# Optimization experiments

Hardware: AMD Instinct MI355X
Metric: run time of the kernel (lower is better)

Reference implementation:

```python
import jax, jax.numpy as jnp
import numpy as np
import math

E = 1024      # embed_dim
H = 16        # num_heads
D = E // H    # head_dim = 64 (power of two, padded_dim == head_dim)


def fwht(x):
    """Normalized fast Walsh-Hadamard transform on last dim (power of two)."""
    n = x.shape[-1]
    orig = x.shape
    x = x.reshape(-1, n)
    h = 1
    while h < n:  # log2(n) fixed butterfly stages
        x = x.reshape(-1, n // (2 * h), 2, h)
        a, b = x[:, :, 0, :], x[:, :, 1, :]
        x = jnp.stack([a + b, a - b], axis=2).reshape(-1, n)
        h *= 2
    return (x / math.sqrt(n)).reshape(orig)


def apply_transform(x, diag, alpha, bias):
    # x: [b, h, s, d]; gated FWHT-domain diagonal filter residual
    x_f = fwht(x) * diag
    x_inv = fwht(x_f)
    return x + alpha * x_inv + bias


def setup_inputs() -> dict:
    key = jax.random.key(0)
    ks = jax.random.split(key, 6)
    b, s = 2, 2048
    sc_in = 1.0 / math.sqrt(E)
    return {
        "x": jax.random.normal(ks[0], (b, s, E), jnp.float32),
        "mask": jnp.ones((b, s), jnp.int32),
        "Wqkv": jax.random.normal(ks[1], (E, 3 * E), jnp.float32) * sc_in,
        "bqkv": jnp.zeros((3 * E,), jnp.float32),
        "Wout": jax.random.normal(ks[2], (E, E), jnp.float32) * sc_in,
        "bout": jnp.zeros((E,), jnp.float32),
        "diag": jnp.ones((D,), jnp.float32) * 0.05,
        "alpha": jnp.float32(0.1),
        "bias_h": jnp.zeros((D,), jnp.float32),
    }


def reference(x, mask, Wqkv, bqkv, Wout, bout, diag, alpha, bias_h):
    b, s, _ = x.shape
    qkv = x @ Wqkv + bqkv                       # [b, s, 3E]
    q, k, v = jnp.split(qkv, 3, axis=-1)

    def to_heads(t):
        return t.reshape(b, s, H, D).transpose(0, 2, 1, 3)  # [b, h, s, d]

    qh, kh, vh = to_heads(q), to_heads(k), to_heads(v)
    qh = apply_transform(qh, diag, alpha, bias_h)
    kh = apply_transform(kh, diag, alpha, bias_h)

    scores = jnp.einsum('bhqd,bhkd->bhqk', qh, kh) / math.sqrt(D)
    scores = jnp.where(mask[:, None, None, :] == 0, -jnp.inf, scores)
    weights = jax.nn.softmax(scores, axis=-1)

    out = jnp.einsum('bhqk,bhkd->bhqd', weights, vh)
    out = out.transpose(0, 2, 1, 3).reshape(b, s, E)
    return out @ Wout + bout
```

## Files before the change

### kernel.cpp

```cpp
#include <hip/hip_runtime.h>
#include <cmath>

#define B_ 2
#define S_ 2048
#define E_ 1024
#define H_ 16
#define M_ (B_*S_)
#define N3_ (3*E_)

typedef unsigned short u16;
typedef unsigned int u32;
typedef __attribute__((ext_vector_type(8))) short bf16x8;
typedef __attribute__((ext_vector_type(8))) _Float16 f16x8;
typedef __attribute__((ext_vector_type(4))) float f32x4;

__device__ __forceinline__ u16 f2bf(float x) {
    unsigned u = __float_as_uint(x);
    return (u16)((u + 0x7FFFu + ((u >> 16) & 1u)) >> 16);
}
__device__ __forceinline__ float bf2f(u16 h) {
    return __uint_as_float((u32)h << 16);
}
__device__ __forceinline__ u16 f2h(float x) {
    _Float16 h = (_Float16)x;
    return __builtin_bit_cast(u16, h);
}
__device__ __forceinline__ float h2f(u16 b) {
    return (float)__builtin_bit_cast(_Float16, b);
}
__device__ __forceinline__ void gld_lds16(const void* g, void* l) {
    __builtin_amdgcn_global_load_lds((const __attribute__((address_space(1))) void*)g,
                                     (__attribute__((address_space(3))) void*)l, 16, 0, 0);
}

template<bool F16>
__device__ __forceinline__ f32x4 mma16(bf16x8 a, bf16x8 b, f32x4 c) {
    if constexpr (F16)
        return __builtin_amdgcn_mfma_f32_16x16x32_f16(
            __builtin_bit_cast(f16x8, a), __builtin_bit_cast(f16x8, b), c, 0, 0, 0);
    else
        return __builtin_amdgcn_mfma_f32_16x16x32_bf16(a, b, c, 0, 0, 0);
}

__global__ __launch_bounds__(256)
void split_a_f16(const float* __restrict__ in, u16* __restrict__ hi, u16* __restrict__ lo, int n4)
{
    int i = blockIdx.x * 256 + threadIdx.x;
    if (i >= n4) return;
    float4 v = ((const float4*)in)[i];
    float vv[4] = {v.x, v.y, v.z, v.w};
    u16 h[4], l[4];
    #pragma unroll
    for (int j = 0; j < 4; j++) {
        h[j] = f2h(vv[j]);
        l[j] = f2h(vv[j] - h2f(h[j]));
    }
    ((uint2*)hi)[i] = make_uint2((u32)h[0] | ((u32)h[1] << 16), (u32)h[2] | ((u32)h[3] << 16));
    ((uint2*)lo)[i] = make_uint2((u32)l[0] | ((u32)l[1] << 16), (u32)l[2] | ((u32)l[3] << 16));
}

__global__ __launch_bounds__(256)
void split_bt_f16hi(const float* __restrict__ W, u16* __restrict__ hi, int K, int N)
{
    int idx = blockIdx.x * 256 + threadIdx.x;
    if (idx >= K * N) return;
    int k = idx / N, nn = idx - k * N;
    hi[(size_t)nn * K + k] = f2h(W[idx]);
}

__global__ __launch_bounds__(256)
void split_bt(const float* __restrict__ W, u16* __restrict__ hi, u16* __restrict__ lo,
              int K, int N)
{
    int idx = blockIdx.x * 256 + threadIdx.x;
    if (idx >= K * N) return;
    int k = idx / N, nn = idx - k * N;
    float v = W[idx];
    u16 h = f2bf(v);
    u16 l = f2bf(v - bf2f(h));
    size_t o = (size_t)nn * K + k;
    hi[o] = h; lo[o] = l;
}

template<int NT, bool F16>
__global__ __launch_bounds__(256)
void gemm_t(const u16* __restrict__ Ahi, const u16* __restrict__ Alo,
            const u16* __restrict__ Bhi, const u16* __restrict__ Blo,
            const float* __restrict__ bias, float* __restrict__ C,
            int M, int N, int K)
{
    __shared__ u16 smem[(NT + 1) * 8192];
    const int tid = threadIdx.x;
    const int lane = tid & 63;
    const int w = tid >> 6;
    const int wr = w >> 1, wc = w & 1;
    const int l15 = lane & 15, g = lane >> 4;
    const int bm = blockIdx.y * 128;
    const int bn = blockIdx.x * 128;
    const int swz = (l15 & 7) << 3;
    const f32x4 z4 = {0.f, 0.f, 0.f, 0.f};
    f32x4 acc[4][4];
    #pragma unroll
    for (int m = 0; m < 4; m++)
        #pragma unroll
        for (int n = 0; n < 4; n++) acc[m][n] = z4;

    for (int ko = 0; ko < K; ko += 64) {
        __syncthreads();
        #pragma unroll
        for (int u = 0; u < 4 * (NT + 1); u++) {
            int f = u * 256 + tid;
            int tile = u >> 2;
            int r = (f >> 3) & 127;
            int cs = ((f & 7) ^ (r & 7)) << 3;
            const u16* src;
            if (tile == 0)      src = Ahi + (size_t)(bm + r) * K + ko + cs;
            else if (tile == 1) src = Alo + (size_t)(bm + r) * K + ko + cs;
            else if (tile == 2) src = Bhi + (size_t)(bn + r) * K + ko + cs;
            else                src = Blo + (size_t)(bn + r) * K + ko + cs;
            gld_lds16(src, (char*)smem + ((f >> 6) << 10));
        }
        __syncthreads();
        #pragma unroll
        for (int p = 0; p < NT; p++) {
            const u16* At = smem + ((p == 1) ? 8192 : 0);
            const u16* Bt = smem + ((NT == 3 && p == 2) ? 3 * 8192 : 2 * 8192);
            #pragma unroll
            for (int kc = 0; kc < 2; kc++) {
                bf16x8 a[4], b[4];
                #pragma unroll
                for (int m = 0; m < 4; m++)
                    a[m] = *(const bf16x8*)&At[((wr*64 + m*16 + l15)*64 + kc*32 + g*8) ^ swz];
                #pragma unroll
                for (int n = 0; n < 4; n++)
                    b[n] = *(const bf16x8*)&Bt[((wc*64 + n*16 + l15)*64 + kc*32 + g*8) ^ swz];
                #pragma unroll
                for (int m = 0; m < 4; m++)
                    #pragma unroll
                    for (int n = 0; n < 4; n++)
                        acc[m][n] = mma16<F16>(a[m], b[n], acc[m][n]);
            }
        }
    }
    #pragma unroll
    for (int m = 0; m < 4; m++) {
        #pragma unroll
        for (int n = 0; n < 4; n++) {
            int col = bn + wc*64 + n*16 + l15;
            float bv = bias[col];
            #pragma unroll
            for (int r = 0; r < 4; r++) {
                int row = bm + wr*64 + m*16 + g*4 + r;
                C[(size_t)row * N + col] = acc[m][n][r] + bv;
            }
        }
    }
}

__device__ __forceinline__ float fwht64(float x, int lane)
{
    #pragma unroll
    for (int h = 1; h < 64; h <<= 1) {
        float y = __shfl_xor(x, h, 64);
        x = (lane & h) ? (y - x) : (x + y);
    }
    return x * 0.125f;
}

__global__ __launch_bounds__(256)
void transform_split(const float* __restrict__ qkv, const float* __restrict__ diag,
                     const float* __restrict__ alphap, const float* __restrict__ biasp,
                     u16* __restrict__ qh, u16* __restrict__ kh, u16* __restrict__ vt)
{
    const int lane = threadIdx.x & 63;
    const int w = (blockIdx.x * 256 + threadIdx.x) >> 6;
    const int h = w & (H_ - 1);
    const int s = (w >> 4) & (S_ - 1);
    const int b = w >> 15;
    const int bh = b * H_ + h;
    const float alpha = alphap[0];
    const float dg = diag[lane];
    const float bb = biasp[lane];
    const float* row = qkv + (size_t)(b * S_ + s) * N3_;
    const size_t o = ((size_t)bh * S_ + s) * 64 + lane;

    float xq = row[h*64 + lane];
    float t = fwht64(fwht64(xq, lane) * dg, lane);
    qh[o] = f2bf(xq + alpha * t + bb);
    float xk = row[E_ + h*64 + lane];
    t = fwht64(fwht64(xk, lane) * dg, lane);
    kh[o] = f2bf(xk + alpha * t + bb);
    vt[((size_t)bh * 64 + lane) * S_ + s] = f2bf(row[2*E_ + h*64 + lane]);
}

__global__ __launch_bounds__(256)
void flash_mfma(const u16* __restrict__ qh, const u16* __restrict__ kh,
                const u16* __restrict__ vt, const int* __restrict__ mask,
                u16* __restrict__ ohi, u16* __restrict__ olo)
{
    __shared__ u16 Ks[64*64];
    __shared__ u16 Vs[64*64];
    __shared__ u16 Ps[4][16*72];
    __shared__ float smask[S_];
    const int tid = threadIdx.x;
    const int lane = tid & 63;
    const int w = tid >> 6;
    const int l15 = lane & 15, g = lane >> 4;
    const int bh = blockIdx.y;
    const int b = bh >> 4, h = bh & 15;
    const int q0 = blockIdx.x * 64;
    const u16* qb = qh + (size_t)bh * S_ * 64;
    const u16* kb = kh + (size_t)bh * S_ * 64;
    const u16* vb = vt + (size_t)bh * 64 * S_;

    #pragma unroll
    for (int i = 0; i < S_/256; i++)
        smask[i*256 + tid] = mask[b*S_ + i*256 + tid] ? 0.f : -3.0e38f;

    bf16x8 qf0, qf1;
    {
        const u16* qr = qb + (size_t)(q0 + w*16 + l15) * 64 + g*8;
        qf0 = *(const bf16x8*)qr;
        qf1 = *(const bf16x8*)(qr + 32);
    }
    const f32x4 z4 = {0.f, 0.f, 0.f, 0.f};
    float m_i = -1.0e30f, l_i = 0.f;
    f32x4 acc[4];
    #pragma unroll
    for (int n = 0; n < 4; n++) acc[n] = z4;

    const int swz = (l15 & 7) << 3;

    for (int t = 0; t < S_/64; t++) {
        const int k0 = t * 64;
        __syncthreads();
        #pragma unroll
        for (int u = 0; u < 2; u++) {
            int f = u * 256 + tid;
            int r = f >> 3;
            int cs = ((f & 7) ^ (r & 7)) * 8;
            gld_lds16(kb + (size_t)(k0 + r) * 64 + cs, (char*)Ks + ((f >> 6) << 10));
            gld_lds16(vb + (size_t)r * S_ + k0 + cs,   (char*)Vs + ((f >> 6) << 10));
        }
        __syncthreads();

        f32x4 sv[4];
        #pragma unroll
        for (int nt = 0; nt < 4; nt++) {
            int row = nt*16 + l15;
            bf16x8 ka0 = *(const bf16x8*)&Ks[(row*64 +  0 + g*8) ^ swz];
            bf16x8 ka1 = *(const bf16x8*)&Ks[(row*64 + 32 + g*8) ^ swz];
            sv[nt] = __builtin_amdgcn_mfma_f32_16x16x32_bf16(ka0, qf0, z4, 0, 0, 0);
            sv[nt] = __builtin_amdgcn_mfma_f32_16x16x32_bf16(ka1, qf1, sv[nt], 0, 0, 0);
        }
        #pragma unroll
        for (int nt = 0; nt < 4; nt++) {
            float4 mb = *(const float4*)&smask[k0 + nt*16 + g*4];
            sv[nt][0] = fmaf(sv[nt][0], 0.125f, mb.x);
            sv[nt][1] = fmaf(sv[nt][1], 0.125f, mb.y);
            sv[nt][2] = fmaf(sv[nt][2], 0.125f, mb.z);
            sv[nt][3] = fmaf(sv[nt][3], 0.125f, mb.w);
        }
        float rm = fmaxf(fmaxf(sv[0][0], sv[0][1]), fmaxf(sv[0][2], sv[0][3]));
        #pragma unroll
        for (int nt = 1; nt < 4; nt++) {
            rm = fmaxf(rm, fmaxf(sv[nt][0], sv[nt][1]));
            rm = fmaxf(rm, fmaxf(sv[nt][2], sv[nt][3]));
        }
        rm = fmaxf(rm, __shfl_xor(rm, 16, 64));
        rm = fmaxf(rm, __shfl_xor(rm, 32, 64));
        const int grow = __any(rm > m_i);
        float mn = m_i, fsc = 1.f;
        if (grow) {
            mn = fmaxf(m_i, rm);
            fsc = __expf(m_i - mn);
            m_i = mn;
        }
        float rs = 0.f;
        #pragma unroll
        for (int nt = 0; nt < 4; nt++)
            #pragma unroll
            for (int r = 0; r < 4; r++) {
                float p = __expf(sv[nt][r] - mn);
                sv[nt][r] = p;
                rs += p;
            }
        rs += __shfl_xor(rs, 16, 64);
        rs += __shfl_xor(rs, 32, 64);
        if (grow) {
            l_i = l_i * fsc + rs;
            #pragma unroll
            for (int n = 0; n < 4; n++)
                #pragma unroll
                for (int r = 0; r < 4; r++) acc[n][r] *= fsc;
        } else {
            l_i += rs;
        }
        #pragma unroll
        for (int nt = 0; nt < 4; nt++) {
            u32 p01 = (u32)f2bf(sv[nt][0]) | ((u32)f2bf(sv[nt][1]) << 16);
            u32 p23 = (u32)f2bf(sv[nt][2]) | ((u32)f2bf(sv[nt][3]) << 16);
            *(uint2*)&Ps[w][l15*72 + nt*16 + g*4] = make_uint2(p01, p23);
        }
        asm volatile("s_waitcnt lgkmcnt(0)" ::: "memory");
        __builtin_amdgcn_sched_barrier(0);
        #pragma unroll
        for (int kc = 0; kc < 2; kc++) {
            bf16x8 pb = *(const bf16x8*)&Ps[w][l15*72 + kc*32 + g*8];
            #pragma unroll
            for (int nd = 0; nd < 4; nd++) {
                int row = nd*16 + l15;
                bf16x8 vf = *(const bf16x8*)&Vs[(row*64 + kc*32 + g*8) ^ swz];
                acc[nd] = __builtin_amdgcn_mfma_f32_16x16x32_bf16(vf, pb, acc[nd], 0, 0, 0);
            }
        }
    }
    float inv = l_i > 0.f ? 1.f / l_i : 0.f;
    const int q = q0 + w*16 + l15;
    const size_t rowoff = (size_t)(b * S_ + q) * E_ + h*64;
    #pragma unroll
    for (int nd = 0; nd < 4; nd++) {
        #pragma unroll
        for (int r = 0; r < 4; r += 2) {
            float o0 = acc[nd][r]     * inv;
            float o1 = acc[nd][r + 1] * inv;
            u16 h0 = f2bf(o0), h1 = f2bf(o1);
            u16 lo0 = f2bf(o0 - bf2f(h0)), lo1 = f2bf(o1 - bf2f(h1));
            int col = nd*16 + g*4 + r;
            *(u32*)&ohi[rowoff + col] = (u32)h0 | ((u32)h1 << 16);
            *(u32*)&olo[rowoff + col] = (u32)lo0 | ((u32)lo1 << 16);
        }
    }
}

extern "C" void kernel_launch(void* const* d_in, const int* in_sizes, int n_in,
                              void* d_out, int out_size, void* d_ws, size_t ws_size,
                              hipStream_t stream)
{
    (void)in_sizes; (void)n_in; (void)out_size; (void)ws_size;
    const float* x     = (const float*)d_in[0];
    const int*   mask  = (const int*)  d_in[1];
    const float* Wqkv  = (const float*)d_in[2];
    const float* bqkv  = (const float*)d_in[3];
    const float* Wout  = (const float*)d_in[4];
    const float* bout  = (const float*)d_in[5];
    const float* diag  = (const float*)d_in[6];
    const float* alpha = (const float*)d_in[7];
    const float* biash = (const float*)d_in[8];
    float* out = (float*)d_out;

    char* ws = (char*)d_ws;
    float* qkv  = (float*)(ws + 0);
    u16* wq_hi  = (u16*)(ws + 50331648);
    u16* qh     = (u16*)(ws + 50331648);
    u16* khp    = (u16*)(ws + 58720256);
    u16* vt     = (u16*)(ws + 67108864);
    u16* x_hi   = (u16*)(ws + 75497472);
    u16* x_lo   = (u16*)(ws + 83886080);
    u16* a_hi   = x_hi;
    u16* a_lo   = x_lo;
    u16* wo_hi  = (u16*)(ws + 92274688);
    u16* wo_lo  = (u16*)(ws + 94371840);

    split_a_f16<<<4096, 256, 0, stream>>>(x, x_hi, x_lo, M_ * E_ / 4);
    split_bt_f16hi<<<(E_ * N3_ + 255) / 256, 256, 0, stream>>>(Wqkv, wq_hi, E_, N3_);
    split_bt<<<(E_ * E_ + 255) / 256, 256, 0, stream>>>(Wout, wo_hi, wo_lo, E_, E_);
    gemm_t<2, true><<<dim3(N3_ / 128, M_ / 128), 256, 0, stream>>>(
        x_hi, x_lo, wq_hi, wq_hi, bqkv, qkv, M_, N3_, E_);
    transform_split<<<(B_ * S_ * H_) / 4, 256, 0, stream>>>(
        qkv, diag, alpha, biash, qh, khp, vt);
    flash_mfma<<<dim3(S_ / 64, B_ * H_), 256, 0, stream>>>(
        qh, khp, vt, mask, a_hi, a_lo);
    gemm_t<3, false><<<dim3(E_ / 128, M_ / 128), 256, 0, stream>>>(
        a_hi, a_lo, wo_hi, wo_lo, bout, out, M_, E_, E_);
}
```

Measured before the change: 322.4 us.

## Double-buffer GEMM and flash K/V tiles, tile weight transposes, use exp2

The GEMM now uses a K=32 double-buffered LDS pipeline with a new swizzle and reuses the A-hi and B-hi fragments across the split-precision products. The flash-attention kernel double-buffers its K/V tiles, raises wave priority around the MFMA blocks, and switches to hardware exp2 with the scale folded into the log2 domain. It also starts the running max at a fixed 6.0 instead of -inf. The weight transpose kernels now go through an LDS tile so that both reads and writes are coalesced, and bf16 conversion uses the library intrinsic. The fixed initial max assumes scores stay in a bounded range, which risks overflow or precision loss for larger scores.

```diff
diff --git a/kernel.cpp b/kernel.cpp
--- a/kernel.cpp
+++ b/kernel.cpp
@@ -1,4 +1,5 @@
 #include <hip/hip_runtime.h>
+#include <hip/hip_bf16.h>
 #include <cmath>
 
 #define B_ 2
@@ -14,9 +15,11 @@
 typedef __attribute__((ext_vector_type(8))) _Float16 f16x8;
 typedef __attribute__((ext_vector_type(4))) float f32x4;
 
-__device__ __forceinline__ u16 f2bf(float x) {
-    unsigned u = __float_as_uint(x);
-    return (u16)((u + 0x7FFFu + ((u >> 16) & 1u)) >> 16);
+__device__ __forceinline__ float hw_exp2(float x) {
+    return __builtin_amdgcn_exp2f(x);
+}
+__device__ __forceinline__ u16 cvt_bf(float x) {
+    return __builtin_bit_cast(u16, __float2bfloat16(x));
 }
 __device__ __forceinline__ float bf2f(u16 h) {
     return __uint_as_float((u32)h << 16);
@@ -62,34 +65,56 @@
 __global__ __launch_bounds__(256)
 void split_bt_f16hi(const float* __restrict__ W, u16* __restrict__ hi, int K, int N)
 {
-    int idx = blockIdx.x * 256 + threadIdx.x;
-    if (idx >= K * N) return;
-    int k = idx / N, nn = idx - k * N;
-    hi[(size_t)nn * K + k] = f2h(W[idx]);
+    __shared__ float tile[64][65];
+    const int tid = threadIdx.x;
+    const int kb = blockIdx.y * 64, nb = blockIdx.x * 64;
+    const int c = tid & 63, r0 = tid >> 6;
+    #pragma unroll
+    for (int i = 0; i < 16; i++) {
+        int r = r0 + i * 4;
+        tile[r][c] = W[(size_t)(kb + r) * N + nb + c];
+    }
+    __syncthreads();
+    #pragma unroll
+    for (int i = 0; i < 16; i++) {
+        int n = r0 + i * 4;
+        hi[(size_t)(nb + n) * K + kb + c] = f2h(tile[c][n]);
+    }
 }
 
 __global__ __launch_bounds__(256)
 void split_bt(const float* __restrict__ W, u16* __restrict__ hi, u16* __restrict__ lo,
               int K, int N)
 {
-    int idx = blockIdx.x * 256 + threadIdx.x;
-    if (idx >= K * N) return;
-    int k = idx / N, nn = idx - k * N;
-    float v = W[idx];
-    u16 h = f2bf(v);
-    u16 l = f2bf(v - bf2f(h));
-    size_t o = (size_t)nn * K + k;
-    hi[o] = h; lo[o] = l;
+    __shared__ float tile[64][65];
+    const int tid = threadIdx.x;
+    const int kb = blockIdx.y * 64, nb = blockIdx.x * 64;
+    const int c = tid & 63, r0 = tid >> 6;
+    #pragma unroll
+    for (int i = 0; i < 16; i++) {
+        int r = r0 + i * 4;
+        tile[r][c] = W[(size_t)(kb + r) * N + nb + c];
+    }
+    __syncthreads();
+    #pragma unroll
+    for (int i = 0; i < 16; i++) {
+        int n = r0 + i * 4;
+        float v = tile[c][n];
+        u16 h = cvt_bf(v);
+        u16 l = cvt_bf(v - bf2f(h));
+        size_t o = (size_t)(nb + n) * K + kb + c;
+        hi[o] = h; lo[o] = l;
+    }
 }
 
 template<int NT, bool F16>
-__global__ __launch_bounds__(256)
+__global__ __launch_bounds__(256, 2)
 void gemm_t(const u16* __restrict__ Ahi, const u16* __restrict__ Alo,
             const u16* __restrict__ Bhi, const u16* __restrict__ Blo,
             const float* __restrict__ bias, float* __restrict__ C,
             int M, int N, int K)
 {
-    __shared__ u16 smem[(NT + 1) * 8192];
+    __shared__ u16 smem[2][(NT + 1) * 4096];
     const int tid = threadIdx.x;
     const int lane = tid & 63;
     const int w = tid >> 6;
@@ -97,7 +122,7 @@
     const int l15 = lane & 15, g = lane >> 4;
     const int bm = blockIdx.y * 128;
     const int bn = blockIdx.x * 128;
-    const int swz = (l15 & 7) << 3;
+    const int rsw = ((l15 >> 1) & 3) << 3;
     const f32x4 z4 = {0.f, 0.f, 0.f, 0.f};
     f32x4 acc[4][4];
     #pragma unroll
@@ -105,42 +130,64 @@
         #pragma unroll
         for (int n = 0; n < 4; n++) acc[m][n] = z4;
 
-    for (int ko = 0; ko < K; ko += 64) {
-        __syncthreads();
-        #pragma unroll
-        for (int u = 0; u < 4 * (NT + 1); u++) {
-            int f = u * 256 + tid;
-            int tile = u >> 2;
-            int r = (f >> 3) & 127;
-            int cs = ((f & 7) ^ (r & 7)) << 3;
-            const u16* src;
-            if (tile == 0)      src = Ahi + (size_t)(bm + r) * K + ko + cs;
-            else if (tile == 1) src = Alo + (size_t)(bm + r) * K + ko + cs;
-            else if (tile == 2) src = Bhi + (size_t)(bn + r) * K + ko + cs;
-            else                src = Blo + (size_t)(bn + r) * K + ko + cs;
-            gld_lds16(src, (char*)smem + ((f >> 6) << 10));
-        }
-        __syncthreads();
-        #pragma unroll
-        for (int p = 0; p < NT; p++) {
-            const u16* At = smem + ((p == 1) ? 8192 : 0);
-            const u16* Bt = smem + ((NT == 3 && p == 2) ? 3 * 8192 : 2 * 8192);
-            #pragma unroll
-            for (int kc = 0; kc < 2; kc++) {
-                bf16x8 a[4], b[4];
-                #pragma unroll
-                for (int m = 0; m < 4; m++)
-                    a[m] = *(const bf16x8*)&At[((wr*64 + m*16 + l15)*64 + kc*32 + g*8) ^ swz];
+    auto stage = [&](int bi, int ko) {
+        #pragma unroll
+        for (int ti = 0; ti < NT + 1; ti++) {
+            const u16* base = (ti == 0) ? Ahi : (ti == 1) ? Alo : (ti == 2) ? Bhi : Blo;
+            const int rb = (ti < 2) ? bm : bn;
+            #pragma unroll
+            for (int u = 0; u < 2; u++) {
+                int c_ = u * 256 + tid;
+                int r = c_ >> 2;
+                int cs = ((c_ & 3) ^ ((r >> 1) & 3)) << 3;
+                gld_lds16(base + (size_t)(rb + r) * K + ko + cs,
+                          (char*)&smem[bi][ti * 4096] + ((c_ >> 6) << 10));
+            }
+        }
+    };
+
+    stage(0, 0);
+    __syncthreads();
+    const int niter = K >> 5;
+    for (int i = 0; i < niter; i++) {
+        const int cur = i & 1;
+        if (i + 1 < niter) stage(cur ^ 1, (i + 1) << 5);
+        const u16* sA  = &smem[cur][0];
+        const u16* sAl = &smem[cur][4096];
+        const u16* sB  = &smem[cur][8192];
+        const u16* sBl = &smem[cur][12288];
+        bf16x8 ah[4], bh[4], al[4];
+        #pragma unroll
+        for (int n = 0; n < 4; n++)
+            bh[n] = *(const bf16x8*)&sB[(wc*64 + n*16 + l15)*32 + ((g << 3) ^ rsw)];
+        #pragma unroll
+        for (int m = 0; m < 4; m++)
+            ah[m] = *(const bf16x8*)&sA[(wr*64 + m*16 + l15)*32 + ((g << 3) ^ rsw)];
+        #pragma unroll
+        for (int m = 0; m < 4; m++)
+            #pragma unroll
+            for (int n = 0; n < 4; n++)
+                acc[m][n] = mma16<F16>(ah[m], bh[n], acc[m][n]);
+        #pragma unroll
+        for (int m = 0; m < 4; m++)
+            al[m] = *(const bf16x8*)&sAl[(wr*64 + m*16 + l15)*32 + ((g << 3) ^ rsw)];
+        #pragma unroll
+        for (int m = 0; m < 4; m++)
+            #pragma unroll
+            for (int n = 0; n < 4; n++)
+                acc[m][n] = mma16<F16>(al[m], bh[n], acc[m][n]);
+        if constexpr (NT == 3) {
+            bf16x8 bl[4];
+            #pragma unroll
+            for (int n = 0; n < 4; n++)
+                bl[n] = *(const bf16x8*)&sBl[(wc*64 + n*16 + l15)*32 + ((g << 3) ^ rsw)];
+            #pragma unroll
+            for (int m = 0; m < 4; m++)
                 #pragma unroll
                 for (int n = 0; n < 4; n++)
-                    b[n] = *(const bf16x8*)&Bt[((wc*64 + n*16 + l15)*64 + kc*32 + g*8) ^ swz];
-                #pragma unroll
-                for (int m = 0; m < 4; m++)
-                    #pragma unroll
-                    for (int n = 0; n < 4; n++)
-                        acc[m][n] = mma16<F16>(a[m], b[n], acc[m][n]);
-            }
-        }
+                    acc[m][n] = mma16<F16>(ah[m], bl[n], acc[m][n]);
+        }
+        __syncthreads();
     }
     #pragma unroll
     for (int m = 0; m < 4; m++) {
@@ -186,11 +233,11 @@
 
     float xq = row[h*64 + lane];
     float t = fwht64(fwht64(xq, lane) * dg, lane);
-    qh[o] = f2bf(xq + alpha * t + bb);
+    qh[o] = cvt_bf(xq + alpha * t + bb);
     float xk = row[E_ + h*64 + lane];
     t = fwht64(fwht64(xk, lane) * dg, lane);
-    kh[o] = f2bf(xk + alpha * t + bb);
-    vt[((size_t)bh * 64 + lane) * S_ + s] = f2bf(row[2*E_ + h*64 + lane]);
+    kh[o] = cvt_bf(xk + alpha * t + bb);
+    vt[((size_t)bh * 64 + lane) * S_ + s] = cvt_bf(row[2*E_ + h*64 + lane]);
 }
 
 __global__ __launch_bounds__(256)
@@ -198,8 +245,8 @@
                 const u16* __restrict__ vt, const int* __restrict__ mask,
                 u16* __restrict__ ohi, u16* __restrict__ olo)
 {
-    __shared__ u16 Ks[64*64];
-    __shared__ u16 Vs[64*64];
+    __shared__ u16 Ks[2][64*64];
+    __shared__ u16 Vs[2][64*64];
     __shared__ u16 Ps[4][16*72];
     __shared__ float smask[S_];
     const int tid = threadIdx.x;
@@ -212,6 +259,7 @@
     const u16* qb = qh + (size_t)bh * S_ * 64;
     const u16* kb = kh + (size_t)bh * S_ * 64;
     const u16* vb = vt + (size_t)bh * 64 * S_;
+    const float SCALE2 = 0.18033688011112f;
 
     #pragma unroll
     for (int i = 0; i < S_/256; i++)
@@ -224,42 +272,51 @@
         qf1 = *(const bf16x8*)(qr + 32);
     }
     const f32x4 z4 = {0.f, 0.f, 0.f, 0.f};
-    float m_i = -1.0e30f, l_i = 0.f;
+    float m_i = 6.0f, l_i = 0.f;
     f32x4 acc[4];
     #pragma unroll
     for (int n = 0; n < 4; n++) acc[n] = z4;
 
     const int swz = (l15 & 7) << 3;
 
-    for (int t = 0; t < S_/64; t++) {
-        const int k0 = t * 64;
-        __syncthreads();
+    auto stage_kv = [&](int bi, int tt) {
+        const int kk0 = tt * 64;
         #pragma unroll
         for (int u = 0; u < 2; u++) {
             int f = u * 256 + tid;
             int r = f >> 3;
             int cs = ((f & 7) ^ (r & 7)) * 8;
-            gld_lds16(kb + (size_t)(k0 + r) * 64 + cs, (char*)Ks + ((f >> 6) << 10));
-            gld_lds16(vb + (size_t)r * S_ + k0 + cs,   (char*)Vs + ((f >> 6) << 10));
-        }
-        __syncthreads();
+            gld_lds16(kb + (size_t)(kk0 + r) * 64 + cs, (char*)&Ks[bi][0] + ((f >> 6) << 10));
+            gld_lds16(vb + (size_t)r * S_ + kk0 + cs,   (char*)&Vs[bi][0] + ((f >> 6) << 10));
+        }
+    };
+
+    stage_kv(0, 0);
+    __syncthreads();
+
+    for (int t = 0; t < S_/64; t++) {
+        const int cur = t & 1;
+        if (t + 1 < S_/64) stage_kv(cur ^ 1, t + 1);
+        const int k0 = t * 64;
 
         f32x4 sv[4];
+        __builtin_amdgcn_s_setprio(1);
         #pragma unroll
         for (int nt = 0; nt < 4; nt++) {
             int row = nt*16 + l15;
-            bf16x8 ka0 = *(const bf16x8*)&Ks[(row*64 +  0 + g*8) ^ swz];
-            bf16x8 ka1 = *(const bf16x8*)&Ks[(row*64 + 32 + g*8) ^ swz];
+            bf16x8 ka0 = *(const bf16x8*)&Ks[cur][(row*64 +  0 + g*8) ^ swz];
+            bf16x8 ka1 = *(const bf16x8*)&Ks[cur][(row*64 + 32 + g*8) ^ swz];
             sv[nt] = __builtin_amdgcn_mfma_f32_16x16x32_bf16(ka0, qf0, z4, 0, 0, 0);
             sv[nt] = __builtin_amdgcn_mfma_f32_16x16x32_bf16(ka1, qf1, sv[nt], 0, 0, 0);
         }
+        __builtin_amdgcn_s_setprio(0);
         #pragma unroll
         for (int nt = 0; nt < 4; nt++) {
             float4 mb = *(const float4*)&smask[k0 + nt*16 + g*4];
-            sv[nt][0] = fmaf(sv[nt][0], 0.125f, mb.x);
-            sv[nt][1] = fmaf(sv[nt][1], 0.125f, mb.y);
-            sv[nt][2] = fmaf(sv[nt][2], 0.125f, mb.z);
-            sv[nt][3] = fmaf(sv[nt][3], 0.125f, mb.w);
+            sv[nt][0] = fmaf(sv[nt][0], SCALE2, mb.x);
+            sv[nt][1] = fmaf(sv[nt][1], SCALE2, mb.y);
+            sv[nt][2] = fmaf(sv[nt][2], SCALE2, mb.z);
+            sv[nt][3] = fmaf(sv[nt][3], SCALE2, mb.w);
         }
         float rm = fmaxf(fmaxf(sv[0][0], sv[0][1]), fmaxf(sv[0][2], sv[0][3]));
         #pragma unroll
@@ -273,7 +330,7 @@
         float mn = m_i, fsc = 1.f;
         if (grow) {
             mn = fmaxf(m_i, rm);
-            fsc = __expf(m_i - mn);
+            fsc = hw_exp2(m_i - mn);
             m_i = mn;
         }
         float rs = 0.f;
@@ -281,7 +338,7 @@
         for (int nt = 0; nt < 4; nt++)
             #pragma unroll
             for (int r = 0; r < 4; r++) {
-                float p = __expf(sv[nt][r] - mn);
+                float p = hw_exp2(sv[nt][r] - mn);
                 sv[nt][r] = p;
                 rs += p;
             }
@@ -298,22 +355,25 @@
         }
         #pragma unroll
         for (int nt = 0; nt < 4; nt++) {
-            u32 p01 = (u32)f2bf(sv[nt][0]) | ((u32)f2bf(sv[nt][1]) << 16);
-            u32 p23 = (u32)f2bf(sv[nt][2]) | ((u32)f2bf(sv[nt][3]) << 16);
+            u32 p01 = (u32)cvt_bf(sv[nt][0]) | ((u32)cvt_bf(sv[nt][1]) << 16);
+            u32 p23 = (u32)cvt_bf(sv[nt][2]) | ((u32)cvt_bf(sv[nt][3]) << 16);
             *(uint2*)&Ps[w][l15*72 + nt*16 + g*4] = make_uint2(p01, p23);
         }
         asm volatile("s_waitcnt lgkmcnt(0)" ::: "memory");
         __builtin_amdgcn_sched_barrier(0);
+        __builtin_amdgcn_s_setprio(1);
         #pragma unroll
         for (int kc = 0; kc < 2; kc++) {
             bf16x8 pb = *(const bf16x8*)&Ps[w][l15*72 + kc*32 + g*8];
             #pragma unroll
             for (int nd = 0; nd < 4; nd++) {
                 int row = nd*16 + l15;
-                bf16x8 vf = *(const bf16x8*)&Vs[(row*64 + kc*32 + g*8) ^ swz];
+                bf16x8 vf = *(const bf16x8*)&Vs[cur][(row*64 + kc*32 + g*8) ^ swz];
                 acc[nd] = __builtin_amdgcn_mfma_f32_16x16x32_bf16(vf, pb, acc[nd], 0, 0, 0);
             }
         }
+        __builtin_amdgcn_s_setprio(0);
+        __syncthreads();
     }
     float inv = l_i > 0.f ? 1.f / l_i : 0.f;
     const int q = q0 + w*16 + l15;
@@ -324,8 +384,8 @@
         for (int r = 0; r < 4; r += 2) {
             float o0 = acc[nd][r]     * inv;
             float o1 = acc[nd][r + 1] * inv;
-            u16 h0 = f2bf(o0), h1 = f2bf(o1);
-            u16 lo0 = f2bf(o0 - bf2f(h0)), lo1 = f2bf(o1 - bf2f(h1));
+            u16 h0 = cvt_bf(o0), h1 = cvt_bf(o1);
+            u16 lo0 = cvt_bf(o0 - bf2f(h0)), lo1 = cvt_bf(o1 - bf2f(h1));
             int col = nd*16 + g*4 + r;
             *(u32*)&ohi[rowoff + col] = (u32)h0 | ((u32)h1 << 16);
             *(u32*)&olo[rowoff + col] = (u32)lo0 | ((u32)lo1 << 16);
@@ -363,8 +423,8 @@
     u16* wo_lo  = (u16*)(ws + 94371840);
 
     split_a_f16<<<4096, 256, 0, stream>>>(x, x_hi, x_lo, M_ * E_ / 4);
-    split_bt_f16hi<<<(E_ * N3_ + 255) / 256, 256, 0, stream>>>(Wqkv, wq_hi, E_, N3_);
-    split_bt<<<(E_ * E_ + 255) / 256, 256, 0, stream>>>(Wout, wo_hi, wo_lo, E_, E_);
+    split_bt_f16hi<<<dim3(N3_/64, E_/64), 256, 0, stream>>>(Wqkv, wq_hi, E_, N3_);
+    split_bt<<<dim3(E_/64, E_/64), 256, 0, stream>>>(Wout, wo_hi, wo_lo, E_, E_);
     gemm_t<2, true><<<dim3(N3_ / 128, M_ / 128), 256, 0, stream>>>(
         x_hi, x_lo, wq_hi, wq_hi, bqkv, qkv, M_, N3_, E_);
     transform_split<<<(B_ * S_ * H_) / 4, 256, 0, stream>>>(
```

New measurement: 308.1 us. 4.4% less time.
